# Optimization experiments

Measured on AMD Instinct MI355X. Metric: run time of the kernel, lower is better.

The kernel has to match this reference:

```python
import jax, jax.numpy as jnp
import numpy as np

B, S, D = 4, 4096, 1024
H, W = 16, 256
DH = D // H


def setup_inputs() -> dict:
    key = jax.random.key(0)
    ks = jax.random.split(key, 5)
    sc = 1.0 / np.sqrt(D)
    return {
        "x": jax.random.normal(ks[0], (B, S, D), jnp.float32),
        "Wq": jax.random.normal(ks[1], (D, D), jnp.float32) * sc,
        "bq": jnp.zeros((D,), jnp.float32),
        "Wk": jax.random.normal(ks[2], (D, D), jnp.float32) * sc,
        "bk": jnp.zeros((D,), jnp.float32),
        "Wv": jax.random.normal(ks[3], (D, D), jnp.float32) * sc,
        "bv": jnp.zeros((D,), jnp.float32),
        "Wo": jax.random.normal(ks[4], (D, D), jnp.float32) * sc,
        "bo": jnp.zeros((D,), jnp.float32),
    }


def reference(x, Wq, bq, Wk, bk, Wv, bv, Wo, bo):
    b, s, d = x.shape
    n = s // W  # seq divisible by window_size -> no padding

    def split_heads(t):
        # (b, s, d) -> (b, h, n, w, dh)
        return t.reshape(b, n, W, H, DH).transpose(0, 3, 1, 2, 4)

    q = split_heads(x @ Wq + bq)
    k = split_heads(x @ Wk + bk)
    v = split_heads(x @ Wv + bv)

    scores = jnp.einsum("bhnqd,bhnkd->bhnqk", q, k) / jnp.sqrt(
        jnp.asarray(DH, x.dtype)
    )
    causal = jnp.tril(jnp.ones((W, W), bool))  # per-block causal mask
    neg = jnp.finfo(scores.dtype).min
    scores = jnp.where(causal, scores, neg)
    weights = jax.nn.softmax(scores, axis=-1)
    out = jnp.einsum("bhnqk,bhnkd->bhnqd", weights, v)
    # (b, h, n, w, dh) -> (b, s, d)
    out = out.transpose(0, 2, 3, 1, 4).reshape(b, s, d)
    return out @ Wo + bo
```

## Files before the change

kernel.cpp:

```cpp
#include <hip/hip_runtime.h>
#include <hip/hip_bf16.h>


typedef __attribute__((ext_vector_type(4))) float f32x4;
typedef __attribute__((ext_vector_type(8))) short s16x8;
typedef __attribute__((ext_vector_type(4))) short s16x4;

__device__ __forceinline__ short f2bf(float f) {
  unsigned u = __float_as_uint(f);
  u += 0x7fffu + ((u >> 16) & 1u);
  return (short)(u >> 16);
}

__device__ __forceinline__ void gload_lds16(const void* g, void* l) {
  __builtin_amdgcn_global_load_lds((const __attribute__((address_space(1))) void*)g,
                                   (__attribute__((address_space(3))) void*)l,
                                   16, 0, 0);
}

__device__ __forceinline__ float rmax16(float v) {
  v = fmaxf(v, __shfl_xor(v, 1, 64));
  v = fmaxf(v, __shfl_xor(v, 2, 64));
  v = fmaxf(v, __shfl_xor(v, 4, 64));
  v = fmaxf(v, __shfl_xor(v, 8, 64));
  return v;
}
__device__ __forceinline__ float rsum16(float v) {
  v += __shfl_xor(v, 1, 64);
  v += __shfl_xor(v, 2, 64);
  v += __shfl_xor(v, 4, 64);
  v += __shfl_xor(v, 8, 64);
  return v;
}

__global__ void cvt_x(const float4* __restrict__ in, s16x4* __restrict__ out, int n4) {
  for (int i = blockIdx.x * 256 + threadIdx.x; i < n4; i += gridDim.x * 256) {
    float4 v = in[i];
    s16x4 o;
    o[0] = f2bf(v.x); o[1] = f2bf(v.y); o[2] = f2bf(v.z); o[3] = f2bf(v.w);
    out[i] = o;
  }
}

__global__ void cvt_wT(const float* __restrict__ W0, const float* __restrict__ W1,
                       const float* __restrict__ W2, const float* __restrict__ W3,
                       short* __restrict__ out) {
  __shared__ float tile[64][65];
  const float* W = (blockIdx.y == 0) ? W0 : (blockIdx.y == 1) ? W1 : (blockIdx.y == 2) ? W2 : W3;
  short* o = out + (size_t)blockIdx.y * (1024 * 1024);
  const int kt = (blockIdx.x >> 4) << 6, nt = (blockIdx.x & 15) << 6;
  const int tid = threadIdx.x;
#pragma unroll
  for (int i = 0; i < 16; ++i) {
    int lin = i * 256 + tid;
    int r = lin >> 6, c = lin & 63;
    tile[r][c] = W[(size_t)(kt + r) * 1024 + nt + c];
  }
  __syncthreads();
#pragma unroll
  for (int i = 0; i < 16; ++i) {
    int lin = i * 256 + tid;
    int r = lin >> 6, c = lin & 63;
    o[(size_t)(nt + r) * 1024 + kt + c] = f2bf(tile[c][r]);
  }
}

template <int NBN, int MODE>
__global__ __launch_bounds__(256) void gemm2(const short* __restrict__ A,
                                             const short* __restrict__ BtBase,
                                             const float* __restrict__ b0,
                                             const float* __restrict__ b1,
                                             const float* __restrict__ b2,
                                             short* __restrict__ Qo,
                                             short* __restrict__ Ko,
                                             short* __restrict__ Vo,
                                             float* __restrict__ Oo) {
  constexpr int Kd = 1024;
  __shared__ short As[2][128 * 32];
  __shared__ short Bs[2][128 * 32];
  const int tid = threadIdx.x;
  const int w = tid >> 6, lane = tid & 63;
  const int d = blockIdx.x;
  const int xcd = d & 7, l = d >> 3;
  constexpr int HALF = NBN * 8;
  const int sub = l / HALF, r = l % HALF;
  const int bn = r >> 3, bm = xcd * 16 + sub * 8 + (r & 7);
  const int m0 = bm << 7, n0 = bn << 7;
  const int wr = (w >> 1) << 6, wc = (w & 1) << 6;
  const int srow = lane >> 2, scol = (lane & 3) << 3;
  const int fr = lane & 15, fk = (lane >> 4) << 3;

  const short* Ab  = A + (size_t)m0 * Kd;
  const short* Btb = BtBase + (size_t)(n0 >> 10) * 1048576 + (size_t)(n0 & 1023) * Kd;

  f32x4 acc[4][4];
#pragma unroll
  for (int i = 0; i < 4; ++i)
#pragma unroll
    for (int j = 0; j < 4; ++j) acc[i][j] = (f32x4){0.f, 0.f, 0.f, 0.f};

#define STAGE(buf, kk)                                                        \
  do {                                                                        \
    _Pragma("unroll") for (int i = 0; i < 2; ++i) {                           \
      const int rr = ((i * 4 + w) << 4) + srow;                               \
      gload_lds16(Ab + (size_t)rr * Kd + (kk) + scol, &As[buf][(i * 4 + w) << 9]); \
      gload_lds16(Btb + (size_t)rr * Kd + (kk) + scol, &Bs[buf][(i * 4 + w) << 9]); \
    }                                                                         \
  } while (0)

  STAGE(0, 0);
  __syncthreads();
  int cur = 0;
#pragma unroll 2
  for (int t = 0; t < 32; ++t) {
    if (t < 31) STAGE(cur ^ 1, (t + 1) << 5);
    s16x8 af[4], bf[4];
#pragma unroll
    for (int mi = 0; mi < 4; ++mi) af[mi] = *(const s16x8*)&As[cur][(wr + mi * 16 + fr) * 32 + fk];
#pragma unroll
    for (int ni = 0; ni < 4; ++ni) bf[ni] = *(const s16x8*)&Bs[cur][(wc + ni * 16 + fr) * 32 + fk];
#pragma unroll
    for (int mi = 0; mi < 4; ++mi)
#pragma unroll
      for (int ni = 0; ni < 4; ++ni)
        acc[mi][ni] = __builtin_amdgcn_mfma_f32_16x16x32_bf16(af[mi], bf[ni], acc[mi][ni], 0, 0, 0);
    __syncthreads();
    cur ^= 1;
  }
#undef STAGE

  const int which = n0 >> 10;
  const float* bb = (which == 0) ? b0 : (which == 1) ? b1 : b2;
  const int col0 = n0 + wc + fr;
  const int row0 = m0 + wr + ((lane >> 4) << 2);
#pragma unroll
  for (int mi = 0; mi < 4; ++mi) {
#pragma unroll
    for (int ni = 0; ni < 4; ++ni) {
      const int c = col0 + ni * 16;
      const float bv = bb[c & 1023];
#pragma unroll
      for (int jj = 0; jj < 4; ++jj) {
        const int rrow = row0 + mi * 16 + jj;
        const float v = acc[mi][ni][jj] + bv;
        if (MODE == 2) {
          Oo[(size_t)rrow * 1024 + c] = v;
        } else {
          const int b = rrow >> 12, s = rrow & 4095;
          const int cl = c & 1023;
          const int h = cl >> 6, dh = cl & 63;
          short* ob = (which == 0) ? Qo : (which == 1) ? Ko : Vo;
          size_t addr;
          if (which < 2) addr = ((size_t)(b * 16 + h) * 4096 + s) * 64 + dh;
          else           addr = ((size_t)(b * 16 + h) * 64 + dh) * 4096 + s;
          ob[addr] = f2bf(v);
        }
      }
    }
  }
}

__global__ __launch_bounds__(256) void attn_kernel(const short* __restrict__ Qg,
                                                   const short* __restrict__ Kg,
                                                   const short* __restrict__ Vg,
                                                   short* __restrict__ AO) {
  constexpr int S = 4096;
  __shared__ short Pl[4][16][272];
  const int tid = threadIdx.x;
  const int w = tid >> 6, lane = tid & 63;
  const int fr = lane & 15, g = lane >> 4;
  const int bhn = blockIdx.x;
  const int nb = bhn & 15, bh = bhn >> 4;
  const int b = bh >> 4, h = bh & 15;
  const short* Qb = Qg + ((size_t)bh * S + nb * 256) * 64;
  const short* Kb = Kg + ((size_t)bh * S + nb * 256) * 64;
  const short* Vb = Vg + (size_t)bh * 64 * S + nb * 256;

#pragma unroll
  for (int qi = 0; qi < 4; ++qi) {
    const int qrow = w * 64 + qi * 16;
    const int dmax = w * 4 + qi;
    const s16x8 aq0 = *(const s16x8*)&Qb[(qrow + fr) * 64 + (g << 3)];
    const s16x8 aq1 = *(const s16x8*)&Qb[(qrow + fr) * 64 + 32 + (g << 3)];
    f32x4 sc[16];
#pragma unroll
    for (int i = 0; i < 16; ++i) sc[i] = (f32x4){0.f, 0.f, 0.f, 0.f};
#pragma unroll
    for (int kt = 0; kt < 16; ++kt) {
      if (kt <= dmax) {
        const s16x8 kf0 = *(const s16x8*)&Kb[(kt * 16 + fr) * 64 + (g << 3)];
        const s16x8 kf1 = *(const s16x8*)&Kb[(kt * 16 + fr) * 64 + 32 + (g << 3)];
        sc[kt] = __builtin_amdgcn_mfma_f32_16x16x32_bf16(aq0, kf0, sc[kt], 0, 0, 0);
        sc[kt] = __builtin_amdgcn_mfma_f32_16x16x32_bf16(aq1, kf1, sc[kt], 0, 0, 0);
      }
    }
    float mrow[4] = {-3e38f, -3e38f, -3e38f, -3e38f};
#pragma unroll
    for (int kt = 0; kt < 16; ++kt) {
      if (kt <= dmax) {
#pragma unroll
        for (int jj = 0; jj < 4; ++jj) {
          float v = sc[kt][jj] * 0.125f;
          if (kt == dmax && fr > (g << 2) + jj) v = -3e38f;
          sc[kt][jj] = v;
          mrow[jj] = fmaxf(mrow[jj], v);
        }
      }
    }
#pragma unroll
    for (int jj = 0; jj < 4; ++jj) mrow[jj] = rmax16(mrow[jj]);
    float lsum[4] = {0.f, 0.f, 0.f, 0.f};
#pragma unroll
    for (int kt = 0; kt < 16; ++kt) {
      if (kt <= dmax) {
#pragma unroll
        for (int jj = 0; jj < 4; ++jj) {
          const float p = __expf(sc[kt][jj] - mrow[jj]);
          sc[kt][jj] = p;
          lsum[jj] += p;
        }
      }
    }
#pragma unroll
    for (int jj = 0; jj < 4; ++jj) lsum[jj] = rsum16(lsum[jj]);
#pragma unroll
    for (int kt = 0; kt < 16; ++kt) {
      if (kt <= dmax) {
#pragma unroll
        for (int jj = 0; jj < 4; ++jj)
          Pl[w][(g << 2) + jj][kt * 16 + fr] = f2bf(sc[kt][jj]);
      } else if (kt == dmax + 1 && ((dmax + 1) & 1)) {
#pragma unroll
        for (int jj = 0; jj < 4; ++jj) Pl[w][(g << 2) + jj][kt * 16 + fr] = 0;
      }
    }
    asm volatile("s_waitcnt lgkmcnt(0)" ::: "memory");
    f32x4 o[4];
#pragma unroll
    for (int di = 0; di < 4; ++di) o[di] = (f32x4){0.f, 0.f, 0.f, 0.f};
    const int nks2 = (dmax + 2) >> 1;
#pragma unroll
    for (int ks2 = 0; ks2 < 8; ++ks2) {
      if (ks2 < nks2) {
        const s16x8 pa = *(const s16x8*)&Pl[w][fr][ks2 * 32 + (g << 3)];
#pragma unroll
        for (int di = 0; di < 4; ++di) {
          const s16x8 vf = *(const s16x8*)&Vb[(size_t)(di * 16 + fr) * S + ks2 * 32 + (g << 3)];
          o[di] = __builtin_amdgcn_mfma_f32_16x16x32_bf16(pa, vf, o[di], 0, 0, 0);
        }
      }
    }
    float inv[4];
#pragma unroll
    for (int jj = 0; jj < 4; ++jj) inv[jj] = 1.f / lsum[jj];
    const int sg = nb * 256 + qrow + (g << 2);
#pragma unroll
    for (int di = 0; di < 4; ++di) {
#pragma unroll
      for (int jj = 0; jj < 4; ++jj) {
        AO[((size_t)b * S + sg + jj) * 1024 + h * 64 + di * 16 + fr] =
            f2bf(o[di][jj] * inv[jj]);
      }
    }
  }
}

extern "C" void kernel_launch(void* const* d_in, const int* in_sizes, int n_in,
                              void* d_out, int out_size, void* d_ws, size_t ws_size,
                              hipStream_t stream) {
  const float* x  = (const float*)d_in[0];
  const float* Wq = (const float*)d_in[1];
  const float* bq = (const float*)d_in[2];
  const float* Wk = (const float*)d_in[3];
  const float* bk = (const float*)d_in[4];
  const float* Wv = (const float*)d_in[5];
  const float* bv = (const float*)d_in[6];
  const float* Wo = (const float*)d_in[7];
  const float* bo = (const float*)d_in[8];
  float* out = (float*)d_out;

  char* ws = (char*)d_ws;
  short* xb  = (short*)ws;
  short* Wt  = (short*)(ws + (size_t)33554432);
  short* Qb  = (short*)(ws + (size_t)33554432 + 8388608);
  short* Kb  = Qb + (size_t)16777216;
  short* Vb  = Kb + (size_t)16777216;
  short* AOb = Vb + (size_t)16777216;

  cvt_x<<<4096, 256, 0, stream>>>((const float4*)x, (s16x4*)xb, 16777216 / 4);
  cvt_wT<<<dim3(256, 4), 256, 0, stream>>>(Wq, Wk, Wv, Wo, Wt);

  gemm2<24, 0><<<3072, 256, 0, stream>>>(xb, Wt, bq, bk, bv, Qb, Kb, Vb, nullptr);

  attn_kernel<<<1024, 256, 0, stream>>>(Qb, Kb, Vb, AOb);

  gemm2<8, 2><<<1024, 256, 0, stream>>>(AOb, Wt + 3145728, bo, bo, bo,
                                        nullptr, nullptr, nullptr, out);
}
```

Baseline: 443.8 us.

## Use 256x256 eight-wave GEMM tiles with swizzled LDS and split attention blocks

Replaces the 128x128 four-wave GEMM with a 256x256 tile computed by eight waves, using a 64-wide K step, XOR-swizzled LDS layout, a four-phase schedule that interleaves async global-to-LDS loads with MFMA bursts, and s_setprio hints. The goal is more data reuse per loaded byte and better overlap of loads with matrix work. The attention kernel now gives each block a quarter of a window, quadrupling the grid to balance the uneven causal work across CUs. The costs are fewer GEMM workgroups (768 and 256), which risks tail imbalance, and higher register pressure from 32 accumulators per wave.

```diff
diff --git a/kernel.cpp b/kernel.cpp
--- a/kernel.cpp
+++ b/kernel.cpp
@@ -66,87 +66,168 @@
 }
 
 template <int NBN, int MODE>
-__global__ __launch_bounds__(256) void gemm2(const short* __restrict__ A,
-                                             const short* __restrict__ BtBase,
-                                             const float* __restrict__ b0,
-                                             const float* __restrict__ b1,
-                                             const float* __restrict__ b2,
-                                             short* __restrict__ Qo,
-                                             short* __restrict__ Ko,
-                                             short* __restrict__ Vo,
-                                             float* __restrict__ Oo) {
-  constexpr int Kd = 1024;
-  __shared__ short As[2][128 * 32];
-  __shared__ short Bs[2][128 * 32];
+__global__ __launch_bounds__(512, 2) void gemm8(const short* __restrict__ A,
+                                                const short* __restrict__ BtBase,
+                                                const float* __restrict__ b0,
+                                                const float* __restrict__ b1,
+                                                const float* __restrict__ b2,
+                                                short* __restrict__ Qo,
+                                                short* __restrict__ Ko,
+                                                short* __restrict__ Vo,
+                                                float* __restrict__ Oo) {
+  __shared__ short As[2][16384];
+  __shared__ short Bs[2][16384];
   const int tid = threadIdx.x;
-  const int w = tid >> 6, lane = tid & 63;
+  const int wid = tid >> 6, lane = tid & 63;
+  const int fr = lane & 15, g = lane >> 4;
+  const int wr = wid >> 2, wc = wid & 3;
+  const int fswz = (fr & 7) << 4;
   const int d = blockIdx.x;
   const int xcd = d & 7, l = d >> 3;
-  constexpr int HALF = NBN * 8;
-  const int sub = l / HALF, r = l % HALF;
-  const int bn = r >> 3, bm = xcd * 16 + sub * 8 + (r & 7);
-  const int m0 = bm << 7, n0 = bn << 7;
-  const int wr = (w >> 1) << 6, wc = (w & 1) << 6;
-  const int srow = lane >> 2, scol = (lane & 3) << 3;
-  const int fr = lane & 15, fk = (lane >> 4) << 3;
-
-  const short* Ab  = A + (size_t)m0 * Kd;
-  const short* Btb = BtBase + (size_t)(n0 >> 10) * 1048576 + (size_t)(n0 & 1023) * Kd;
-
-  f32x4 acc[4][4];
-#pragma unroll
-  for (int i = 0; i < 4; ++i)
+  const int bm = xcd * 8 + l / NBN, bn = l % NBN;
+  const int m0 = bm << 8, n0 = bn << 8;
+  const int which = n0 >> 10;
+  const char* Ab = (const char*)(A + (size_t)m0 * 1024);
+  const char* Bb = (const char*)(BtBase + (size_t)which * 1048576 + (size_t)(n0 & 1023) * 1024);
+
+  const int srow = tid >> 3;
+  const int kb = ((tid & 7) << 4) ^ ((srow & 7) << 4);
+  const char* aSrc = Ab + (size_t)srow * 2048 + kb;
+  const char* bSrc = Bb + (size_t)srow * 2048 + kb;
+  const int ldsOff = wid << 10;
+
+#define STAGE2(srcp, dstp, i0, tt)                                            \
+  do {                                                                        \
+    gload_lds16((srcp) + (size_t)(i0) * 131072 + (size_t)(tt) * 128,          \
+                (dstp) + (i0) * 8192 + ldsOff);                               \
+    gload_lds16((srcp) + (size_t)((i0) + 1) * 131072 + (size_t)(tt) * 128,    \
+                (dstp) + ((i0) + 1) * 8192 + ldsOff);                         \
+  } while (0)
+
+#define AFRAG(mi, ks) (*(const s16x8*)(Acur + ((((wr) << 7) + (mi) * 16 + fr) << 7) + \
+                                       ((((ks) << 6) | (g << 4)) ^ fswz)))
+#define BFRAG(ni, ks) (*(const s16x8*)(Bcur + ((((wc) << 6) + (ni) * 16 + fr) << 7) + \
+                                       ((((ks) << 6) | (g << 4)) ^ fswz)))
+
+#define PHASE_MID()                                       \
+  __builtin_amdgcn_s_barrier();                           \
+  asm volatile("s_waitcnt lgkmcnt(0)" ::: "memory");      \
+  __builtin_amdgcn_sched_barrier(0);                      \
+  __builtin_amdgcn_s_setprio(1)
+
+#define PHASE_END()                                       \
+  __builtin_amdgcn_s_setprio(0);                          \
+  __builtin_amdgcn_s_barrier()
+
+  f32x4 acc[8][4];
+#pragma unroll
+  for (int i = 0; i < 8; ++i)
 #pragma unroll
     for (int j = 0; j < 4; ++j) acc[i][j] = (f32x4){0.f, 0.f, 0.f, 0.f};
 
-#define STAGE(buf, kk)                                                        \
-  do {                                                                        \
-    _Pragma("unroll") for (int i = 0; i < 2; ++i) {                           \
-      const int rr = ((i * 4 + w) << 4) + srow;                               \
-      gload_lds16(Ab + (size_t)rr * Kd + (kk) + scol, &As[buf][(i * 4 + w) << 9]); \
-      gload_lds16(Btb + (size_t)rr * Kd + (kk) + scol, &Bs[buf][(i * 4 + w) << 9]); \
-    }                                                                         \
-  } while (0)
-
-  STAGE(0, 0);
-  __syncthreads();
-  int cur = 0;
+  {
+    char* A0 = (char*)&As[0][0];
+    char* B0 = (char*)&Bs[0][0];
+    STAGE2(aSrc, A0, 0, 0); STAGE2(aSrc, A0, 2, 0);
+    STAGE2(bSrc, B0, 0, 0); STAGE2(bSrc, B0, 2, 0);
+  }
+
 #pragma unroll 2
-  for (int t = 0; t < 32; ++t) {
-    if (t < 31) STAGE(cur ^ 1, (t + 1) << 5);
-    s16x8 af[4], bf[4];
-#pragma unroll
-    for (int mi = 0; mi < 4; ++mi) af[mi] = *(const s16x8*)&As[cur][(wr + mi * 16 + fr) * 32 + fk];
-#pragma unroll
-    for (int ni = 0; ni < 4; ++ni) bf[ni] = *(const s16x8*)&Bs[cur][(wc + ni * 16 + fr) * 32 + fk];
-#pragma unroll
-    for (int mi = 0; mi < 4; ++mi)
-#pragma unroll
-      for (int ni = 0; ni < 4; ++ni)
-        acc[mi][ni] = __builtin_amdgcn_mfma_f32_16x16x32_bf16(af[mi], bf[ni], acc[mi][ni], 0, 0, 0);
-    __syncthreads();
-    cur ^= 1;
-  }
-#undef STAGE
-
-  const int which = n0 >> 10;
+  for (int t = 0; t < 16; ++t) {
+    const int cur = t & 1;
+    const int tn = t + 1;
+    const bool pre = (t < 15);
+    const char* Acur = (const char*)&As[cur][0];
+    const char* Bcur = (const char*)&Bs[cur][0];
+    char* Anxt = (char*)&As[cur ^ 1][0];
+    char* Bnxt = (char*)&Bs[cur ^ 1][0];
+
+    asm volatile("s_waitcnt vmcnt(0)" ::: "memory");
+    __builtin_amdgcn_s_barrier();
+
+    s16x8 aF[2][4], bF0[2][2], bF1[2][2];
+#pragma unroll
+    for (int ks = 0; ks < 2; ++ks) {
+#pragma unroll
+      for (int mi = 0; mi < 4; ++mi) aF[ks][mi] = AFRAG(mi, ks);
+#pragma unroll
+      for (int ni = 0; ni < 2; ++ni) bF0[ks][ni] = BFRAG(ni, ks);
+    }
+    if (pre) STAGE2(aSrc, Anxt, 0, tn);
+    PHASE_MID();
+#pragma unroll
+    for (int ks = 0; ks < 2; ++ks)
+#pragma unroll
+      for (int mi = 0; mi < 4; ++mi)
+#pragma unroll
+        for (int ni = 0; ni < 2; ++ni)
+          acc[mi][ni] = __builtin_amdgcn_mfma_f32_16x16x32_bf16(aF[ks][mi], bF0[ks][ni], acc[mi][ni], 0, 0, 0);
+    PHASE_END();
+
+#pragma unroll
+    for (int ks = 0; ks < 2; ++ks)
+#pragma unroll
+      for (int ni = 0; ni < 2; ++ni) bF1[ks][ni] = BFRAG(2 + ni, ks);
+    if (pre) STAGE2(aSrc, Anxt, 2, tn);
+    PHASE_MID();
+#pragma unroll
+    for (int ks = 0; ks < 2; ++ks)
+#pragma unroll
+      for (int mi = 0; mi < 4; ++mi)
+#pragma unroll
+        for (int ni = 0; ni < 2; ++ni)
+          acc[mi][2 + ni] = __builtin_amdgcn_mfma_f32_16x16x32_bf16(aF[ks][mi], bF1[ks][ni], acc[mi][2 + ni], 0, 0, 0);
+    PHASE_END();
+
+#pragma unroll
+    for (int ks = 0; ks < 2; ++ks)
+#pragma unroll
+      for (int mi = 0; mi < 4; ++mi) aF[ks][mi] = AFRAG(4 + mi, ks);
+    if (pre) STAGE2(bSrc, Bnxt, 0, tn);
+    PHASE_MID();
+#pragma unroll
+    for (int ks = 0; ks < 2; ++ks)
+#pragma unroll
+      for (int mi = 0; mi < 4; ++mi)
+#pragma unroll
+        for (int ni = 0; ni < 2; ++ni)
+          acc[4 + mi][2 + ni] = __builtin_amdgcn_mfma_f32_16x16x32_bf16(aF[ks][mi], bF1[ks][ni], acc[4 + mi][2 + ni], 0, 0, 0);
+    PHASE_END();
+
+    if (pre) STAGE2(bSrc, Bnxt, 2, tn);
+    PHASE_MID();
+#pragma unroll
+    for (int ks = 0; ks < 2; ++ks)
+#pragma unroll
+      for (int mi = 0; mi < 4; ++mi)
+#pragma unroll
+        for (int ni = 0; ni < 2; ++ni)
+          acc[4 + mi][ni] = __builtin_amdgcn_mfma_f32_16x16x32_bf16(aF[ks][mi], bF0[ks][ni], acc[4 + mi][ni], 0, 0, 0);
+    PHASE_END();
+  }
+#undef STAGE2
+#undef AFRAG
+#undef BFRAG
+#undef PHASE_MID
+#undef PHASE_END
+
   const float* bb = (which == 0) ? b0 : (which == 1) ? b1 : b2;
-  const int col0 = n0 + wc + fr;
-  const int row0 = m0 + wr + ((lane >> 4) << 2);
-#pragma unroll
-  for (int mi = 0; mi < 4; ++mi) {
+  const int row0 = m0 + wr * 128 + (g << 2);
+  const int col0 = n0 + wc * 64 + fr;
+#pragma unroll
+  for (int mi = 0; mi < 8; ++mi) {
 #pragma unroll
     for (int ni = 0; ni < 4; ++ni) {
       const int c = col0 + ni * 16;
       const float bv = bb[c & 1023];
 #pragma unroll
       for (int jj = 0; jj < 4; ++jj) {
-        const int rrow = row0 + mi * 16 + jj;
+        const int r = row0 + mi * 16 + jj;
         const float v = acc[mi][ni][jj] + bv;
         if (MODE == 2) {
-          Oo[(size_t)rrow * 1024 + c] = v;
+          Oo[(size_t)r * 1024 + c] = v;
         } else {
-          const int b = rrow >> 12, s = rrow & 4095;
+          const int b = r >> 12, s = r & 4095;
           const int cl = c & 1023;
           const int h = cl >> 6, dh = cl & 63;
           short* ob = (which == 0) ? Qo : (which == 1) ? Ko : Vo;
@@ -169,98 +250,96 @@
   const int tid = threadIdx.x;
   const int w = tid >> 6, lane = tid & 63;
   const int fr = lane & 15, g = lane >> 4;
-  const int bhn = blockIdx.x;
-  const int nb = bhn & 15, bh = bhn >> 4;
+  const int idx = blockIdx.x;
+  const int qq = idx & 3;
+  const int nb = (idx >> 2) & 15, bh = idx >> 6;
   const int b = bh >> 4, h = bh & 15;
   const short* Qb = Qg + ((size_t)bh * S + nb * 256) * 64;
   const short* Kb = Kg + ((size_t)bh * S + nb * 256) * 64;
   const short* Vb = Vg + (size_t)bh * 64 * S + nb * 256;
 
-#pragma unroll
-  for (int qi = 0; qi < 4; ++qi) {
-    const int qrow = w * 64 + qi * 16;
-    const int dmax = w * 4 + qi;
-    const s16x8 aq0 = *(const s16x8*)&Qb[(qrow + fr) * 64 + (g << 3)];
-    const s16x8 aq1 = *(const s16x8*)&Qb[(qrow + fr) * 64 + 32 + (g << 3)];
-    f32x4 sc[16];
-#pragma unroll
-    for (int i = 0; i < 16; ++i) sc[i] = (f32x4){0.f, 0.f, 0.f, 0.f};
-#pragma unroll
-    for (int kt = 0; kt < 16; ++kt) {
-      if (kt <= dmax) {
-        const s16x8 kf0 = *(const s16x8*)&Kb[(kt * 16 + fr) * 64 + (g << 3)];
-        const s16x8 kf1 = *(const s16x8*)&Kb[(kt * 16 + fr) * 64 + 32 + (g << 3)];
-        sc[kt] = __builtin_amdgcn_mfma_f32_16x16x32_bf16(aq0, kf0, sc[kt], 0, 0, 0);
-        sc[kt] = __builtin_amdgcn_mfma_f32_16x16x32_bf16(aq1, kf1, sc[kt], 0, 0, 0);
+  const int qrow = qq * 64 + w * 16;
+  const int dmax = qq * 4 + w;
+  const s16x8 aq0 = *(const s16x8*)&Qb[(qrow + fr) * 64 + (g << 3)];
+  const s16x8 aq1 = *(const s16x8*)&Qb[(qrow + fr) * 64 + 32 + (g << 3)];
+  f32x4 sc[16];
+#pragma unroll
+  for (int i = 0; i < 16; ++i) sc[i] = (f32x4){0.f, 0.f, 0.f, 0.f};
+#pragma unroll
+  for (int kt = 0; kt < 16; ++kt) {
+    if (kt <= dmax) {
+      const s16x8 kf0 = *(const s16x8*)&Kb[(kt * 16 + fr) * 64 + (g << 3)];
+      const s16x8 kf1 = *(const s16x8*)&Kb[(kt * 16 + fr) * 64 + 32 + (g << 3)];
+      sc[kt] = __builtin_amdgcn_mfma_f32_16x16x32_bf16(aq0, kf0, sc[kt], 0, 0, 0);
+      sc[kt] = __builtin_amdgcn_mfma_f32_16x16x32_bf16(aq1, kf1, sc[kt], 0, 0, 0);
+    }
+  }
+  float mrow[4] = {-3e38f, -3e38f, -3e38f, -3e38f};
+#pragma unroll
+  for (int kt = 0; kt < 16; ++kt) {
+    if (kt <= dmax) {
+#pragma unroll
+      for (int jj = 0; jj < 4; ++jj) {
+        float v = sc[kt][jj] * 0.125f;
+        if (kt == dmax && fr > (g << 2) + jj) v = -3e38f;
+        sc[kt][jj] = v;
+        mrow[jj] = fmaxf(mrow[jj], v);
       }
     }
-    float mrow[4] = {-3e38f, -3e38f, -3e38f, -3e38f};
-#pragma unroll
-    for (int kt = 0; kt < 16; ++kt) {
-      if (kt <= dmax) {
-#pragma unroll
-        for (int jj = 0; jj < 4; ++jj) {
-          float v = sc[kt][jj] * 0.125f;
-          if (kt == dmax && fr > (g << 2) + jj) v = -3e38f;
-          sc[kt][jj] = v;
-          mrow[jj] = fmaxf(mrow[jj], v);
-        }
+  }
+#pragma unroll
+  for (int jj = 0; jj < 4; ++jj) mrow[jj] = rmax16(mrow[jj]);
+  float lsum[4] = {0.f, 0.f, 0.f, 0.f};
+#pragma unroll
+  for (int kt = 0; kt < 16; ++kt) {
+    if (kt <= dmax) {
+#pragma unroll
+      for (int jj = 0; jj < 4; ++jj) {
+        const float p = __expf(sc[kt][jj] - mrow[jj]);
+        sc[kt][jj] = p;
+        lsum[jj] += p;
       }
     }
-#pragma unroll
-    for (int jj = 0; jj < 4; ++jj) mrow[jj] = rmax16(mrow[jj]);
-    float lsum[4] = {0.f, 0.f, 0.f, 0.f};
-#pragma unroll
-    for (int kt = 0; kt < 16; ++kt) {
-      if (kt <= dmax) {
-#pragma unroll
-        for (int jj = 0; jj < 4; ++jj) {
-          const float p = __expf(sc[kt][jj] - mrow[jj]);
-          sc[kt][jj] = p;
-          lsum[jj] += p;
-        }
+  }
+#pragma unroll
+  for (int jj = 0; jj < 4; ++jj) lsum[jj] = rsum16(lsum[jj]);
+#pragma unroll
+  for (int kt = 0; kt < 16; ++kt) {
+    if (kt <= dmax) {
+#pragma unroll
+      for (int jj = 0; jj < 4; ++jj)
+        Pl[w][(g << 2) + jj][kt * 16 + fr] = f2bf(sc[kt][jj]);
+    } else if (kt == dmax + 1 && ((dmax + 1) & 1)) {
+#pragma unroll
+      for (int jj = 0; jj < 4; ++jj) Pl[w][(g << 2) + jj][kt * 16 + fr] = 0;
+    }
+  }
+  asm volatile("s_waitcnt lgkmcnt(0)" ::: "memory");
+  f32x4 o[4];
+#pragma unroll
+  for (int di = 0; di < 4; ++di) o[di] = (f32x4){0.f, 0.f, 0.f, 0.f};
+  const int nks2 = (dmax + 2) >> 1;
+#pragma unroll
+  for (int ks2 = 0; ks2 < 8; ++ks2) {
+    if (ks2 < nks2) {
+      const s16x8 pa = *(const s16x8*)&Pl[w][fr][ks2 * 32 + (g << 3)];
+#pragma unroll
+      for (int di = 0; di < 4; ++di) {
+        const s16x8 vf = *(const s16x8*)&Vb[(size_t)(di * 16 + fr) * S + ks2 * 32 + (g << 3)];
+        o[di] = __builtin_amdgcn_mfma_f32_16x16x32_bf16(pa, vf, o[di], 0, 0, 0);
       }
     }
-#pragma unroll
-    for (int jj = 0; jj < 4; ++jj) lsum[jj] = rsum16(lsum[jj]);
-#pragma unroll
-    for (int kt = 0; kt < 16; ++kt) {
-      if (kt <= dmax) {
-#pragma unroll
-        for (int jj = 0; jj < 4; ++jj)
-          Pl[w][(g << 2) + jj][kt * 16 + fr] = f2bf(sc[kt][jj]);
-      } else if (kt == dmax + 1 && ((dmax + 1) & 1)) {
-#pragma unroll
-        for (int jj = 0; jj < 4; ++jj) Pl[w][(g << 2) + jj][kt * 16 + fr] = 0;
-      }
-    }
-    asm volatile("s_waitcnt lgkmcnt(0)" ::: "memory");
-    f32x4 o[4];
-#pragma unroll
-    for (int di = 0; di < 4; ++di) o[di] = (f32x4){0.f, 0.f, 0.f, 0.f};
-    const int nks2 = (dmax + 2) >> 1;
-#pragma unroll
-    for (int ks2 = 0; ks2 < 8; ++ks2) {
-      if (ks2 < nks2) {
-        const s16x8 pa = *(const s16x8*)&Pl[w][fr][ks2 * 32 + (g << 3)];
-#pragma unroll
-        for (int di = 0; di < 4; ++di) {
-          const s16x8 vf = *(const s16x8*)&Vb[(size_t)(di * 16 + fr) * S + ks2 * 32 + (g << 3)];
-          o[di] = __builtin_amdgcn_mfma_f32_16x16x32_bf16(pa, vf, o[di], 0, 0, 0);
-        }
-      }
-    }
-    float inv[4];
-#pragma unroll
-    for (int jj = 0; jj < 4; ++jj) inv[jj] = 1.f / lsum[jj];
-    const int sg = nb * 256 + qrow + (g << 2);
-#pragma unroll
-    for (int di = 0; di < 4; ++di) {
-#pragma unroll
-      for (int jj = 0; jj < 4; ++jj) {
-        AO[((size_t)b * S + sg + jj) * 1024 + h * 64 + di * 16 + fr] =
-            f2bf(o[di][jj] * inv[jj]);
-      }
+  }
+  float inv[4];
+#pragma unroll
+  for (int jj = 0; jj < 4; ++jj) inv[jj] = 1.f / lsum[jj];
+  const int sg = nb * 256 + qrow + (g << 2);
+#pragma unroll
+  for (int di = 0; di < 4; ++di) {
+#pragma unroll
+    for (int jj = 0; jj < 4; ++jj) {
+      AO[((size_t)b * S + sg + jj) * 1024 + h * 64 + di * 16 + fr] =
+          f2bf(o[di][jj] * inv[jj]);
     }
   }
 }
@@ -290,10 +369,10 @@
   cvt_x<<<4096, 256, 0, stream>>>((const float4*)x, (s16x4*)xb, 16777216 / 4);
   cvt_wT<<<dim3(256, 4), 256, 0, stream>>>(Wq, Wk, Wv, Wo, Wt);
 
-  gemm2<24, 0><<<3072, 256, 0, stream>>>(xb, Wt, bq, bk, bv, Qb, Kb, Vb, nullptr);
-
-  attn_kernel<<<1024, 256, 0, stream>>>(Qb, Kb, Vb, AOb);
-
-  gemm2<8, 2><<<1024, 256, 0, stream>>>(AOb, Wt + 3145728, bo, bo, bo,
-                                        nullptr, nullptr, nullptr, out);
-}
+  gemm8<12, 0><<<768, 512, 0, stream>>>(xb, Wt, bq, bk, bv, Qb, Kb, Vb, nullptr);
+
+  attn_kernel<<<4096, 256, 0, stream>>>(Qb, Kb, Vb, AOb);
+
+  gemm8<4, 2><<<256, 512, 0, stream>>>(AOb, Wt + 3145728, bo, bo, bo,
+                                       nullptr, nullptr, nullptr, out);
+}
```

After: 481.6 us. 8.5% more time.
